# Kernel optimization log

Measured on AMD Instinct MI355X. Metric: run time of the kernel, lower is better.

## Reference

```python
import jax, jax.numpy as jnp
import numpy as np

B, C, J, T, S = 16, 4, 19, 256, 10
D1, D2, DS, O = 64, 64, 128, 64  # embed hidden, embed out, similarity dim, out channels
EPS = 1e-5


def setup_inputs() -> dict:
    key = jax.random.key(0)
    ks = jax.random.split(key, 12)
    sc = 0.05
    return {
        'x': jax.random.normal(ks[0], (B, C, J, T, S), dtype=jnp.float32),
        'gamma': jnp.ones((C * J * T,), dtype=jnp.float32),
        'beta': jnp.zeros((C * J * T,), dtype=jnp.float32),
        'w1': jax.random.normal(ks[1], (D1, C), dtype=jnp.float32) * sc,
        'b1': jax.random.normal(ks[2], (D1,), dtype=jnp.float32) * sc,
        'w2': jax.random.normal(ks[3], (D2, D1), dtype=jnp.float32) * sc,
        'b2': jax.random.normal(ks[4], (D2,), dtype=jnp.float32) * sc,
        'ws1': jax.random.normal(ks[5], (DS, D2), dtype=jnp.float32) * sc,
        'bs1': jax.random.normal(ks[6], (DS,), dtype=jnp.float32) * sc,
        'ws2': jax.random.normal(ks[7], (DS, D2), dtype=jnp.float32) * sc,
        'bs2': jax.random.normal(ks[8], (DS,), dtype=jnp.float32) * sc,
        'W': jax.random.normal(ks[9], (D2, O), dtype=jnp.float32) * sc,
    }


def _bn(x, gamma, beta):
    # BatchNorm1d in training mode on x viewed as (B, C*J*T, S): stats over (batch, step)
    b, c, j, t, s = x.shape
    xf = x.reshape(b, c * j * t, s)
    mean = xf.mean(axis=(0, 2), keepdims=True)
    var = ((xf - mean) ** 2).mean(axis=(0, 2), keepdims=True)
    xn = (xf - mean) * jax.lax.rsqrt(var + EPS)
    xn = xn * gamma[None, :, None] + beta[None, :, None]
    return xn.reshape(b, c, j, t, s)


def _conv1x1(x, w, bias):
    # Conv3d with kernel 1 == channel mix: (B,Cin,J,T,S) x (Cout,Cin)
    y = jnp.einsum('bcjts,oc->bojts', x, w)
    return y + bias[None, :, None, None, None]


def reference(x, gamma, beta, w1, b1, w2, b2, ws1, bs1, ws2, bs2, W):
    # embed: norm -> 1x1 conv -> relu -> 1x1 conv -> relu
    h = _bn(x, gamma, beta)
    h = jax.nn.relu(_conv1x1(h, w1, b1))
    h = jax.nn.relu(_conv1x1(h, w2, b2))  # (B, 64, J, T, S)
    # compute_similarity: learned dense adjacency over joints per (b, s, t)
    s1 = _conv1x1(h, ws1, bs1)  # (B, 128, J, T, S)
    s2 = _conv1x1(h, ws2, bs2)
    logits = jnp.einsum('bcjts,bckts->bstjk', s1, s2)  # (B, S, T, J, J)
    att = jax.nn.softmax(logits, axis=-1)
    # aggregate node features then mix channels with weight (64, O)
    agg = jnp.einsum('bstjk,bckts->bstjc', att, h)  # (B, S, T, J, 64)
    out = jnp.einsum('bstjc,co->bojts', agg, W)  # (B, O, J, T, S)
    return out
```

## Files before the change

### kernel.cpp

```cpp
#include <hip/hip_runtime.h>
#include <hip/hip_bf16.h>

#define B_   16
#define C_   4
#define J_   19
#define T_   256
#define S_   10
#define JT_  4864
#define CJT_ 19456

#define WS_SCALE 0
#define WS_SHIFT 19456
#define WS_Q2    38912
#define WS_F16_BYTE ((38912 + 64) * 4)
#define H_W2 0
#define H_Q  4096
#define H_WT 8192

typedef _Float16 f16;
typedef _Float16 half8 __attribute__((ext_vector_type(8)));
typedef _Float16 f16x4 __attribute__((ext_vector_type(4)));
typedef float f32x4 __attribute__((ext_vector_type(4)));

__device__ __forceinline__ float bf2f(__hip_bfloat16 v) { return __bfloat162float(v); }
__device__ __forceinline__ float bfbits2f(unsigned short u) {
    unsigned int w = ((unsigned int)u) << 16;
    return __builtin_bit_cast(float, w);
}
__device__ __forceinline__ float ldin(const void* p, int i, bool f32) {
    if (f32) return ((const float*)p)[i];
    return bf2f(((const __hip_bfloat16*)p)[i]);
}
__device__ __forceinline__ bool dtype_is_f32(const void* gamma) {
    return ((const unsigned short*)gamma)[0] == 0;
}
__device__ __forceinline__ f32x4 mfma16(half8 a, half8 b, f32x4 c) {
    return __builtin_amdgcn_mfma_f32_16x16x32_f16(a, b, c, 0, 0, 0);
}
__device__ __forceinline__ int swz64(int row, int col) {
    return (row << 6) + ((((col >> 3) ^ (row & 7)) << 3)) + (col & 7);
}

extern "C" __global__ __launch_bounds__(1024)
void setup_kernel(const void* __restrict__ x, const void* __restrict__ gamma,
                  const void* __restrict__ beta, const void* __restrict__ w2,
                  const void* __restrict__ ws1, const void* __restrict__ ws2,
                  const void* __restrict__ bs1, const void* __restrict__ Wm,
                  float* __restrict__ wsf)
{
    const bool f32 = dtype_is_f32(gamma);
    const int tid = threadIdx.x;
    __shared__ float redS[4][256], redQ[4][256];

    if (blockIdx.x < 76) {
        const int cj = blockIdx.x;
        const int t  = tid & 255;
        const int bq = tid >> 8;
        float sum = 0.f, sq = 0.f;
        for (int bb = 0; bb < 4; ++bb) {
            int b = bq * 4 + bb;
            size_t base = ((size_t)(b * 76 + cj)) * 2560 + (size_t)t * 10;
            float va[10];
            if (f32) {
                __builtin_memcpy(va, (const float*)x + base, 40);
            } else {
                unsigned short ua[10];
                __builtin_memcpy(ua, (const unsigned short*)x + base, 20);
#pragma unroll
                for (int k = 0; k < 10; ++k) va[k] = bfbits2f(ua[k]);
            }
#pragma unroll
            for (int k = 0; k < 10; ++k) {
                sum += va[k];
                sq  = fmaf(va[k], va[k], sq);
            }
        }
        redS[bq][t] = sum;
        redQ[bq][t] = sq;
        __syncthreads();
        if (bq == 0) {
            sum = redS[0][t] + redS[1][t] + redS[2][t] + redS[3][t];
            sq  = redQ[0][t] + redQ[1][t] + redQ[2][t] + redQ[3][t];
            int ch = cj * 256 + t;
            float mean = sum * (1.f / 160.f);
            float var  = fmaxf(sq * (1.f / 160.f) - mean * mean, 0.f);
            float scl = ldin(gamma, ch, f32) * rsqrtf(var + 1e-5f);
            wsf[WS_SCALE + ch] = scl;
            wsf[WS_SHIFT + ch] = ldin(beta, ch, f32) - mean * scl;
        }
        return;
    }

    f16* hws = (f16*)((char*)wsf + WS_F16_BYTE);
    int id = (blockIdx.x - 76) * 1024 + tid;
    if (id < 4096) {
        int a = id >> 6, b = id & 63;
        float acc = 0.f;
        for (int ds = 0; ds < 128; ++ds)
            acc = fmaf(ldin(ws1, ds * 64 + a, f32), ldin(ws2, ds * 64 + b, f32), acc);
        hws[H_Q + id] = (f16)acc;
    } else if (id < 8192) {
        int i = id - 4096;
        hws[H_W2 + i] = (f16)ldin(w2, i, f32);
    } else if (id < 12288) {
        int i = id - 8192;
        int o = i >> 6, c = i & 63;
        hws[H_WT + i] = (f16)ldin(Wm, c * 64 + o, f32);
    } else if (id < 12352) {
        int b = id - 12288;
        float acc = 0.f;
        for (int ds = 0; ds < 128; ++ds)
            acc = fmaf(ldin(ws2, ds * 64 + b, f32), ldin(bs1, ds, f32), acc);
        wsf[WS_Q2 + b] = acc;
    }
}

#define HWSTR 116
#define ATSTR 40

#define R1_OFF 0
#define R2_OFF 14848
#define R3_OFF 29184
#define R4_OFF 43520
#define XNR_OFF (R4_OFF)
#define W1F_OFF (R4_OFF + 1600)
#define B1F_OFF (R4_OFF + 2624)
#define B2F_OFF (R4_OFF + 2880)
#define Q2F_OFF (R4_OFF + 3136)
#define LOG_OFF (R4_OFF)
#define VBH_OFF (R4_OFF + 3616)
#define ARENA_BYTES 47360

extern "C" __global__ __launch_bounds__(256, 3)
void fused_kernel(const void* __restrict__ x,
                  const void* __restrict__ w1, const void* __restrict__ b1,
                  const void* __restrict__ b2, const void* __restrict__ gamma,
                  const float* __restrict__ wsf, void* __restrict__ outv)
{
    const bool f32o = dtype_is_f32(gamma);
    const int tid = threadIdx.x;
    const int lane = tid & 63;
    const int wave = tid >> 6;
    const int l15 = lane & 15;
    const int q4 = lane >> 4;

    const int hw  = blockIdx.x;
    const int bid = (hw & 7) * 1024 + (hw >> 3);
    const int b  = bid >> 9;
    const int t  = (bid >> 1) & 255;
    const int sh = bid & 1;

    __shared__ __align__(16) unsigned char arena[ARENA_BYTES];

    f16* h1row  = (f16*)(arena + R1_OFF);
    f16* hWT    = (f16*)(arena + R1_OFF);
    f16* h2row  = (f16*)(arena + R2_OFF);
    f16* outb   = (f16*)(arena + R2_OFF);
    f16* urow   = (f16*)(arena + R3_OFF);
    f16* att    = (f16*)(arena + R3_OFF);
    f16* logits = (f16*)(arena + LOG_OFF);
    f16* vbh    = (f16*)(arena + VBH_OFF);
    float* xnr  = (float*)(arena + XNR_OFF);
    float* w1f  = (float*)(arena + W1F_OFF);
    float* b1f  = (float*)(arena + B1F_OFF);
    float* b2f  = (float*)(arena + B2F_OFF);
    float* q2f  = (float*)(arena + Q2F_OFF);

    const f16* hws = (const f16*)((const char*)wsf + WS_F16_BYTE);

    w1f[tid] = ldin(w1, tid, f32o);
    if (tid < 64) {
        b1f[tid] = ldin(b1, tid, f32o);
        b2f[tid] = ldin(b2, tid, f32o);
        q2f[tid] = wsf[WS_Q2 + tid];
    }
    for (int e = tid; e < 400; e += 256) {
        int R = e >> 2, c = e & 3;
        int sL = R / 20, j = R - sL * 20;
        float val = 0.f;
        if (j < 19) {
            int sg = sh * 5 + sL;
            int xidx = ((b * 4 + c) * 19 + j) * 2560 + t * 10 + sg;
            int ch = (c * 19 + j) * 256 + t;
            val = ldin(x, xidx, f32o) * wsf[WS_SCALE + ch] + wsf[WS_SHIFT + ch];
        }
        xnr[e] = val;
    }
    __syncthreads();

    {
        int d = tid & 63;
        float4 wr = *(const float4*)&w1f[d * 4];
        float bb = b1f[d];
        for (int r = 0; r < 25; ++r) {
            int R = wave * 25 + r;
            float4 xc = *(const float4*)&xnr[R * 4];
            float h = fmaf(xc.x, wr.x, fmaf(xc.y, wr.y, fmaf(xc.z, wr.z, fmaf(xc.w, wr.w, bb))));
            h1row[swz64(R, d)] = (f16)fmaxf(h, 0.f);
        }
    }
    __syncthreads();

#define LDFRAG(base, row0, stride, koff) \
    (*(const half8*)((base) + ((row0) + l15) * (stride) + (koff) + (q4 << 3)))
#define LDSWZ(base, row0, koff) \
    (*(const half8*)((base) + (((row0) + l15) << 6) + \
        ((((((koff) >> 3) + q4) ^ (((row0) + l15) & 7)) << 3))))

    {
        int n0 = wave * 16;
        half8 B0 = LDFRAG(hws + H_W2, n0, 64, 0);
        half8 B1 = LDFRAG(hws + H_W2, n0, 64, 32);
        float bias = b2f[n0 + l15];
        for (int m = 0; m < 7; ++m) {
            half8 A0 = LDSWZ(h1row, m * 16, 0);
            half8 A1 = LDSWZ(h1row, m * 16, 32);
            f32x4 c = {bias, bias, bias, bias};
            c = mfma16(A0, B0, c);
            c = mfma16(A1, B1, c);
#pragma unroll
            for (int i = 0; i < 4; ++i) {
                int r = m * 16 + q4 * 4 + i;
                h2row[swz64(r, n0 + l15)] = (f16)fmaxf(c[i], 0.f);
            }
        }
    }
    __syncthreads();

    {
        int n0 = wave * 16;
        half8 B0 = LDFRAG(hws + H_Q, n0, 64, 0);
        half8 B1 = LDFRAG(hws + H_Q, n0, 64, 32);
        for (int m = 0; m < 7; ++m) {
            half8 A0 = LDSWZ(h2row, m * 16, 0);
            half8 A1 = LDSWZ(h2row, m * 16, 32);
            f32x4 c = {0.f, 0.f, 0.f, 0.f};
            c = mfma16(A0, B0, c);
            c = mfma16(A1, B1, c);
#pragma unroll
            for (int i = 0; i < 4; ++i) {
                int r = m * 16 + q4 * 4 + i;
                urow[swz64(r, n0 + l15)] = (f16)c[i];
            }
        }
        if (tid < 100) {
            const f16* hr = &h2row[tid << 6];
            float acc = 0.f;
#pragma unroll
            for (int g = 0; g < 8; ++g) {
                half8 hv = *(const half8*)&hr[(g ^ (tid & 7)) << 3];
#pragma unroll
                for (int jj = 0; jj < 8; ++jj)
                    acc = fmaf((float)hv[jj], q2f[g * 8 + jj], acc);
            }
            vbh[tid] = (f16)acc;
        }
    }
    __syncthreads();

    {
        for (int e = tid; e < 64 * 21; e += 256) {
            int o = e / 21, zi = e - o * 21;
            int col = (zi < 4) ? (zi * 20 + 19) : (zi + 95);
            hWT[o * HWSTR + col] = (f16)0.f;
        }
        int n0 = wave * 16;
        half8 B0 = LDFRAG(hws + H_WT, n0, 64, 0);
        half8 B1 = LDFRAG(hws + H_WT, n0, 64, 32);
        for (int m = 0; m < 7; ++m) {
            half8 A0 = LDSWZ(h2row, m * 16, 0);
            half8 A1 = LDSWZ(h2row, m * 16, 32);
            f32x4 c = {0.f, 0.f, 0.f, 0.f};
            c = mfma16(A0, B0, c);
            c = mfma16(A1, B1, c);
#pragma unroll
            for (int i = 0; i < 4; ++i) {
                int r = m * 16 + q4 * 4 + i;
                int s = r / 20, j = r - s * 20;
                if (r < 100 && j < 19)
                    hWT[(n0 + l15) * HWSTR + r] = (f16)c[i];
            }
        }
        for (int task = wave; task < 10; task += 4) {
            int s = task >> 1, nt = task & 1;
            int n0g = s * 20 + nt * 16;
            half8 Bb0 = LDSWZ(urow, n0g, 0);
            half8 Bb1 = LDSWZ(urow, n0g, 32);
            int kloc = nt * 16 + l15;
            bool kval = kloc < 19;
            float vv = (float)vbh[s * 20 + ((kloc < 19) ? kloc : 0)];
#pragma unroll
            for (int mt = 0; mt < 2; ++mt) {
                int m0 = s * 20 + mt * 16;
                half8 A0 = LDSWZ(h2row, m0, 0);
                half8 A1 = LDSWZ(h2row, m0, 32);
                f32x4 c = {0.f, 0.f, 0.f, 0.f};
                c = mfma16(A0, Bb0, c);
                c = mfma16(A1, Bb1, c);
#pragma unroll
                for (int i = 0; i < 4; ++i) {
                    int j = mt * 16 + q4 * 4 + i;
                    if (j < 19 && kval)
                        logits[s * 361 + j * 19 + kloc] = (f16)(c[i] + vv);
                }
            }
        }
    }
    __syncthreads();

    if (tid < 95) {
        int sL = tid / 19, j = tid - sL * 19;
        int R = sL * 20 + j;
        const f16* lp = logits + sL * 361 + j * 19;
        float lv[19];
#pragma unroll
        for (int k = 0; k < 19; ++k) lv[k] = (float)lp[k];
        float m = lv[0];
#pragma unroll
        for (int k = 1; k < 19; ++k) m = fmaxf(m, lv[k]);
        float e[19], sum = 0.f;
#pragma unroll
        for (int k = 0; k < 19; ++k) { e[k] = __expf(lv[k] - m); sum += e[k]; }
        float rs = 1.f / sum;
        half8 H[4];
#pragma unroll
        for (int g = 0; g < 4; ++g)
#pragma unroll
            for (int k = 0; k < 8; ++k) {
                int idx = g * 8 + k;
                H[g][k] = (idx < 19) ? (f16)(e[idx] * rs) : (f16)0.f;
            }
        f16* ap = &att[R * ATSTR];
#pragma unroll
        for (int g = 0; g < 4; ++g)
            *(half8*)(ap + g * 8) = H[g];
    }
    __syncthreads();

    for (int task = wave; task < 20; task += 4) {
        int s = task >> 2, nt = task & 3;
        int o0 = nt * 16;
        const f16* bp = &hWT[(o0 + l15) * HWSTR + s * 20 + (q4 << 3)];
        f16x4 blo = *(const f16x4*)bp;
        f16x4 bhi = *(const f16x4*)(bp + 4);
        half8 Bf = __builtin_shufflevector(blo, bhi, 0, 1, 2, 3, 4, 5, 6, 7);
#pragma unroll
        for (int mt = 0; mt < 2; ++mt) {
            int m0 = s * 20 + mt * 16;
            half8 Af = *(const half8*)&att[(m0 + l15) * ATSTR + (q4 << 3)];
            f32x4 c = {0.f, 0.f, 0.f, 0.f};
            c = mfma16(Af, Bf, c);
#pragma unroll
            for (int i = 0; i < 4; ++i) {
                int j = mt * 16 + q4 * 4 + i;
                if (j < 19)
                    outb[swz64(s * 19 + j, o0 + l15)] = (f16)c[i];
            }
        }
    }
    __syncthreads();

    for (int p = 0; p < 5; ++p) {
        int id = p * 256 + tid;
        if (id < 1216) {
            int o = id / 19, j = id - o * 19;
            int obase = ((b * 64 + o) * 19 + j) * 2560 + t * 10 + sh * 5;
            if (f32o) {
                float tmp[5];
#pragma unroll
                for (int sl = 0; sl < 5; ++sl)
                    tmp[sl] = (float)outb[swz64(sl * 19 + j, o)];
                __builtin_memcpy((float*)outv + obase, tmp, 20);
            } else {
                unsigned short tmp[5];
#pragma unroll
                for (int sl = 0; sl < 5; ++sl) {
                    __hip_bfloat16 h = __float2bfloat16((float)outb[swz64(sl * 19 + j, o)]);
                    tmp[sl] = __builtin_bit_cast(unsigned short, h);
                }
                __builtin_memcpy((__hip_bfloat16*)outv + obase, tmp, 10);
            }
        }
    }
}

extern "C" void kernel_launch(void* const* d_in, const int* in_sizes, int n_in,
                              void* d_out, int out_size, void* d_ws, size_t ws_size,
                              hipStream_t stream)
{
    const void* x     = d_in[0];
    const void* gamma = d_in[1];
    const void* beta  = d_in[2];
    const void* w1    = d_in[3];
    const void* b1    = d_in[4];
    const void* w2    = d_in[5];
    const void* b2    = d_in[6];
    const void* ws1   = d_in[7];
    const void* bs1   = d_in[8];
    const void* ws2   = d_in[9];
    const void* bs2   = d_in[10];
    const void* Wm    = d_in[11];
    float* wsf = (float*)d_ws;

    hipLaunchKernelGGL(setup_kernel, dim3(89), dim3(1024), 0, stream,
                       x, gamma, beta, w2, ws1, ws2, bs1, Wm, wsf);
    hipLaunchKernelGGL(fused_kernel, dim3(B_ * T_ * 2), dim3(256), 0, stream,
                       x, w1, b1, b2, gamma, wsf, d_out);
}
```

Baseline: 406.2 us.

## Move first 1x1 conv onto MFMA and pack joint rows densely

The scalar FMA loop for the first channel-mix conv is replaced by an MFMA with a zero-padded fp16 w1 fragment, which setup_kernel now precomputes. Rows are packed at 19 per step instead of padded to 20, so the MFMA row-tile loops shrink from 7 to 6 iterations. The shared-memory staging of w1, b1, b2 and q2 is removed to cut LDS use and barriers, and those values are read directly from global memory. In exchange the normalized input is rounded to fp16 before the first conv, and the attention tiles now read across step boundaries, which depends on the zero padding and masking being correct.

New measurement: 393.7 us. -3.1%, faster.

```diff
diff --git a/kernel.cpp b/kernel.cpp
--- a/kernel.cpp
+++ b/kernel.cpp
@@ -16,6 +16,7 @@
 #define H_W2 0
 #define H_Q  4096
 #define H_WT 8192
+#define H_W1 12288
 
 typedef _Float16 f16;
 typedef _Float16 half8 __attribute__((ext_vector_type(8)));
@@ -43,7 +44,8 @@
 
 extern "C" __global__ __launch_bounds__(1024)
 void setup_kernel(const void* __restrict__ x, const void* __restrict__ gamma,
-                  const void* __restrict__ beta, const void* __restrict__ w2,
+                  const void* __restrict__ beta, const void* __restrict__ w1,
+                  const void* __restrict__ w2,
                   const void* __restrict__ ws1, const void* __restrict__ ws2,
                   const void* __restrict__ bs1, const void* __restrict__ Wm,
                   float* __restrict__ wsf)
@@ -112,29 +114,29 @@
         for (int ds = 0; ds < 128; ++ds)
             acc = fmaf(ldin(ws2, ds * 64 + b, f32), ldin(bs1, ds, f32), acc);
         wsf[WS_Q2 + b] = acc;
+    } else if (id < 14400) {
+        int i = id - 12352;
+        int d = i >> 5, k = i & 31;
+        hws[H_W1 + i] = (k < 4) ? (f16)ldin(w1, d * 4 + k, f32) : (f16)0.f;
     }
 }
 
 #define HWSTR 116
 #define ATSTR 40
+#define XSTR  40
 
 #define R1_OFF 0
 #define R2_OFF 14848
-#define R3_OFF 29184
-#define R4_OFF 43520
-#define XNR_OFF (R4_OFF)
-#define W1F_OFF (R4_OFF + 1600)
-#define B1F_OFF (R4_OFF + 2624)
-#define B2F_OFF (R4_OFF + 2880)
-#define Q2F_OFF (R4_OFF + 3136)
+#define R3_OFF 27136
+#define R4_OFF 39424
 #define LOG_OFF (R4_OFF)
 #define VBH_OFF (R4_OFF + 3616)
-#define ARENA_BYTES 47360
+#define ARENA_BYTES 47104
 
 extern "C" __global__ __launch_bounds__(256, 3)
 void fused_kernel(const void* __restrict__ x,
-                  const void* __restrict__ w1, const void* __restrict__ b1,
-                  const void* __restrict__ b2, const void* __restrict__ gamma,
+                  const void* __restrict__ b1, const void* __restrict__ b2,
+                  const void* __restrict__ gamma,
                   const float* __restrict__ wsf, void* __restrict__ outv)
 {
     const bool f32o = dtype_is_f32(gamma);
@@ -158,46 +160,27 @@
     f16* outb   = (f16*)(arena + R2_OFF);
     f16* urow   = (f16*)(arena + R3_OFF);
     f16* att    = (f16*)(arena + R3_OFF);
+    f16* xnr16  = (f16*)(arena + R4_OFF);
     f16* logits = (f16*)(arena + LOG_OFF);
     f16* vbh    = (f16*)(arena + VBH_OFF);
-    float* xnr  = (float*)(arena + XNR_OFF);
-    float* w1f  = (float*)(arena + W1F_OFF);
-    float* b1f  = (float*)(arena + B1F_OFF);
-    float* b2f  = (float*)(arena + B2F_OFF);
-    float* q2f  = (float*)(arena + Q2F_OFF);
 
     const f16* hws = (const f16*)((const char*)wsf + WS_F16_BYTE);
 
-    w1f[tid] = ldin(w1, tid, f32o);
-    if (tid < 64) {
-        b1f[tid] = ldin(b1, tid, f32o);
-        b2f[tid] = ldin(b2, tid, f32o);
-        q2f[tid] = wsf[WS_Q2 + tid];
-    }
-    for (int e = tid; e < 400; e += 256) {
-        int R = e >> 2, c = e & 3;
-        int sL = R / 20, j = R - sL * 20;
-        float val = 0.f;
-        if (j < 19) {
+    for (int v = tid; v < 480; v += 256) {
+        int R = v / 5, g = v - R * 5;
+        half8 z = {(f16)0.f, (f16)0.f, (f16)0.f, (f16)0.f,
+                   (f16)0.f, (f16)0.f, (f16)0.f, (f16)0.f};
+        if (g == 0 && R < 95) {
+            int sL = R / 19, j = R - sL * 19;
             int sg = sh * 5 + sL;
-            int xidx = ((b * 4 + c) * 19 + j) * 2560 + t * 10 + sg;
-            int ch = (c * 19 + j) * 256 + t;
-            val = ldin(x, xidx, f32o) * wsf[WS_SCALE + ch] + wsf[WS_SHIFT + ch];
-        }
-        xnr[e] = val;
-    }
-    __syncthreads();
-
-    {
-        int d = tid & 63;
-        float4 wr = *(const float4*)&w1f[d * 4];
-        float bb = b1f[d];
-        for (int r = 0; r < 25; ++r) {
-            int R = wave * 25 + r;
-            float4 xc = *(const float4*)&xnr[R * 4];
-            float h = fmaf(xc.x, wr.x, fmaf(xc.y, wr.y, fmaf(xc.z, wr.z, fmaf(xc.w, wr.w, bb))));
-            h1row[swz64(R, d)] = (f16)fmaxf(h, 0.f);
-        }
+#pragma unroll
+            for (int c = 0; c < 4; ++c) {
+                int xidx = ((b * 4 + c) * 19 + j) * 2560 + t * 10 + sg;
+                int ch = (c * 19 + j) * 256 + t;
+                z[c] = (f16)(ldin(x, xidx, f32o) * wsf[WS_SCALE + ch] + wsf[WS_SHIFT + ch]);
+            }
+        }
+        *(half8*)&xnr16[R * XSTR + (g << 3)] = z;
     }
     __syncthreads();
 
@@ -209,10 +192,27 @@
 
     {
         int n0 = wave * 16;
+        half8 Bw = LDFRAG(hws + H_W1, n0, 32, 0);
+        float bias = ldin(b1, n0 + l15, f32o);
+        for (int m = 0; m < 6; ++m) {
+            half8 Af = *(const half8*)&xnr16[(m * 16 + l15) * XSTR + (q4 << 3)];
+            f32x4 c = {bias, bias, bias, bias};
+            c = mfma16(Af, Bw, c);
+#pragma unroll
+            for (int i = 0; i < 4; ++i) {
+                int r = m * 16 + q4 * 4 + i;
+                h1row[swz64(r, n0 + l15)] = (f16)fmaxf(c[i], 0.f);
+            }
+        }
+    }
+    __syncthreads();
+
+    {
+        int n0 = wave * 16;
         half8 B0 = LDFRAG(hws + H_W2, n0, 64, 0);
         half8 B1 = LDFRAG(hws + H_W2, n0, 64, 32);
-        float bias = b2f[n0 + l15];
-        for (int m = 0; m < 7; ++m) {
+        float bias = ldin(b2, n0 + l15, f32o);
+        for (int m = 0; m < 6; ++m) {
             half8 A0 = LDSWZ(h1row, m * 16, 0);
             half8 A1 = LDSWZ(h1row, m * 16, 32);
             f32x4 c = {bias, bias, bias, bias};
@@ -231,7 +231,7 @@
         int n0 = wave * 16;
         half8 B0 = LDFRAG(hws + H_Q, n0, 64, 0);
         half8 B1 = LDFRAG(hws + H_Q, n0, 64, 32);
-        for (int m = 0; m < 7; ++m) {
+        for (int m = 0; m < 6; ++m) {
             half8 A0 = LDSWZ(h2row, m * 16, 0);
             half8 A1 = LDSWZ(h2row, m * 16, 32);
             f32x4 c = {0.f, 0.f, 0.f, 0.f};
@@ -243,7 +243,7 @@
                 urow[swz64(r, n0 + l15)] = (f16)c[i];
             }
         }
-        if (tid < 100) {
+        if (tid < 95) {
             const f16* hr = &h2row[tid << 6];
             float acc = 0.f;
 #pragma unroll
@@ -251,7 +251,7 @@
                 half8 hv = *(const half8*)&hr[(g ^ (tid & 7)) << 3];
 #pragma unroll
                 for (int jj = 0; jj < 8; ++jj)
-                    acc = fmaf((float)hv[jj], q2f[g * 8 + jj], acc);
+                    acc = fmaf((float)hv[jj], wsf[WS_Q2 + g * 8 + jj], acc);
             }
             vbh[tid] = (f16)acc;
         }
@@ -261,13 +261,13 @@
     {
         for (int e = tid; e < 64 * 21; e += 256) {
             int o = e / 21, zi = e - o * 21;
-            int col = (zi < 4) ? (zi * 20 + 19) : (zi + 95);
+            int col = (zi < 5) ? (zi * 20 + 19) : (95 + zi);
             hWT[o * HWSTR + col] = (f16)0.f;
         }
         int n0 = wave * 16;
         half8 B0 = LDFRAG(hws + H_WT, n0, 64, 0);
         half8 B1 = LDFRAG(hws + H_WT, n0, 64, 32);
-        for (int m = 0; m < 7; ++m) {
+        for (int m = 0; m < 6; ++m) {
             half8 A0 = LDSWZ(h2row, m * 16, 0);
             half8 A1 = LDSWZ(h2row, m * 16, 32);
             f32x4 c = {0.f, 0.f, 0.f, 0.f};
@@ -276,22 +276,23 @@
 #pragma unroll
             for (int i = 0; i < 4; ++i) {
                 int r = m * 16 + q4 * 4 + i;
-                int s = r / 20, j = r - s * 20;
-                if (r < 100 && j < 19)
-                    hWT[(n0 + l15) * HWSTR + r] = (f16)c[i];
+                if (r < 95) {
+                    int s = r / 19;
+                    hWT[(n0 + l15) * HWSTR + r + s] = (f16)c[i];
+                }
             }
         }
         for (int task = wave; task < 10; task += 4) {
             int s = task >> 1, nt = task & 1;
-            int n0g = s * 20 + nt * 16;
+            int n0g = s * 19 + nt * 16;
             half8 Bb0 = LDSWZ(urow, n0g, 0);
             half8 Bb1 = LDSWZ(urow, n0g, 32);
             int kloc = nt * 16 + l15;
             bool kval = kloc < 19;
-            float vv = (float)vbh[s * 20 + ((kloc < 19) ? kloc : 0)];
+            float vv = (float)vbh[s * 19 + ((kloc < 19) ? kloc : 0)];
 #pragma unroll
             for (int mt = 0; mt < 2; ++mt) {
-                int m0 = s * 20 + mt * 16;
+                int m0 = s * 19 + mt * 16;
                 half8 A0 = LDSWZ(h2row, m0, 0);
                 half8 A1 = LDSWZ(h2row, m0, 32);
                 f32x4 c = {0.f, 0.f, 0.f, 0.f};
@@ -310,7 +311,6 @@
 
     if (tid < 95) {
         int sL = tid / 19, j = tid - sL * 19;
-        int R = sL * 20 + j;
         const f16* lp = logits + sL * 361 + j * 19;
         float lv[19];
 #pragma unroll
@@ -330,7 +330,7 @@
                 int idx = g * 8 + k;
                 H[g][k] = (idx < 19) ? (f16)(e[idx] * rs) : (f16)0.f;
             }
-        f16* ap = &att[R * ATSTR];
+        f16* ap = &att[tid * ATSTR];
 #pragma unroll
         for (int g = 0; g < 4; ++g)
             *(half8*)(ap + g * 8) = H[g];
@@ -346,7 +346,7 @@
         half8 Bf = __builtin_shufflevector(blo, bhi, 0, 1, 2, 3, 4, 5, 6, 7);
 #pragma unroll
         for (int mt = 0; mt < 2; ++mt) {
-            int m0 = s * 20 + mt * 16;
+            int m0 = s * 19 + mt * 16;
             half8 Af = *(const half8*)&att[(m0 + l15) * ATSTR + (q4 << 3)];
             f32x4 c = {0.f, 0.f, 0.f, 0.f};
             c = mfma16(Af, Bf, c);
@@ -402,8 +402,8 @@
     const void* Wm    = d_in[11];
     float* wsf = (float*)d_ws;
 
-    hipLaunchKernelGGL(setup_kernel, dim3(89), dim3(1024), 0, stream,
-                       x, gamma, beta, w2, ws1, ws2, bs1, Wm, wsf);
+    hipLaunchKernelGGL(setup_kernel, dim3(91), dim3(1024), 0, stream,
+                       x, gamma, beta, w1, w2, ws1, ws2, bs1, Wm, wsf);
     hipLaunchKernelGGL(fused_kernel, dim3(B_ * T_ * 2), dim3(256), 0, stream,
-                       x, w1, b1, b2, gamma, wsf, d_out);
-}
+                       x, b1, b2, gamma, wsf, d_out);
+}
```
